# Optimization experiments

Hardware: AMD Instinct MI355X
Metric: run time of the kernel (lower is better)

## Reference

```python
import jax, jax.numpy as jnp
import numpy as np

N_SAMPLE = 1000
N_LATENT = 64
N_OUT = 64
BATCH = 65536


def setup_inputs() -> dict:
    key = jax.random.key(0)
    k_u, k_sid, k_A, k_off = jax.random.split(key, 4)
    u = jax.random.normal(k_u, (BATCH, N_LATENT), dtype=jnp.float32)
    sample_id = jax.random.randint(k_sid, (BATCH, 1), 0, N_SAMPLE, dtype=jnp.int64)
    amat_sample = jax.random.normal(k_A, (N_SAMPLE, N_LATENT, N_OUT), dtype=jnp.float32)
    offsets = jax.random.normal(k_off, (N_SAMPLE, N_OUT), dtype=jnp.float32)
    return {"u": u, "sample_id": sample_id, "amat_sample": amat_sample, "offsets": offsets}


def reference(u, sample_id, amat_sample, offsets):
    # sample_id: [B, 1] -> [B]
    sid = jnp.squeeze(sample_id, axis=-1).astype(jnp.int32)
    # Gather per-cell decoder matrix: [B, n_latent, n_out]
    As = amat_sample[sid]
    # Original detaches u before the matvec (gradient only flows via residual).
    u_sg = jax.lax.stop_gradient(u)
    # Batched matvec: (As * u[..., None]).sum(-2)
    z2 = jnp.einsum('bd,bdo->bo', u_sg, As)
    delta = z2 + offsets[sid]
    return u + delta
```

## Files before the change

kernel.cpp:

```cpp
#include <hip/hip_runtime.h>
#include <hip/hip_bf16.h>

#define N_LATENT 64
#define N_OUT    64
#define CAP      256
#define CSTRIDE  16
#define NWAVES   5
#define TPAD     68

typedef __attribute__((ext_vector_type(8))) _Float16 f16x8;
typedef __attribute__((ext_vector_type(4))) float    f32x4;

union U4H8 { uint4 u4; f16x8 h8; };

__global__ __launch_bounds__(256) void build_lists_kernel(
    const int* __restrict__ sid,
    int* __restrict__ cursor,
    int* __restrict__ list,
    int batch)
{
    const int i = blockIdx.x * blockDim.x + threadIdx.x;
    if (i < batch) {
        const int s = sid[i];
        const int p = atomicAdd(&cursor[s * CSTRIDE], 1);
        if (p < CAP) list[s * CAP + p] = i;
    }
}

__global__ __launch_bounds__(64 * NWAVES) void decoder_mfma_kernel(
    const float* __restrict__ u,
    const float* __restrict__ amat,
    const float* __restrict__ offsets,
    const int*   __restrict__ cursor,
    const int*   __restrict__ list,
    float*       __restrict__ out)
{
    __shared__ uint  Bf[8 * 64 * 4];
    __shared__ float Ot[NWAVES][16 * TPAD];

    const int s    = blockIdx.x;
    const int tid  = threadIdx.x;
    const int lane = tid & 63;
    const int wave = tid >> 6;

    int n = cursor[s * CSTRIDE];
    n = (n < CAP) ? n : CAP;
    if (n == 0) return;

    const float* __restrict__ Ag  = amat + (size_t)s * (N_LATENT * N_OUT);
    const int*   __restrict__ lst = list + s * CAP;

    for (int c = wave; c < 8; c += NWAVES) {
        const int kk  = c >> 2;
        const int nt  = c & 3;
        const int kb  = kk * 32 + (lane >> 4) * 8;
        const int col = nt * 16 + (lane & 15);
        U4H8 x;
#pragma unroll
        for (int j = 0; j < 8; ++j)
            x.h8[j] = (_Float16)Ag[(kb + j) * N_OUT + col];
        *((uint4*)&Bf[(c * 64 + lane) * 4]) = x.u4;
    }
    __syncthreads();

    const int tiles = (n + 15) >> 4;

    const float4 offv = *(const float4*)(offsets + (size_t)s * N_OUT + (lane & 15) * 4);

    float* __restrict__ myT = &Ot[wave][0];

    for (int t = wave; t < tiles; t += NWAVES) {
        const int ridx = t * 16 + (lane & 15);
        const int brow = lst[(ridx < n) ? ridx : 0];
        const float* __restrict__ up =
            u + (size_t)brow * N_LATENT + ((lane >> 4) * 8);
        f16x8 a0, a1;
        {
            const float4 p0 = *(const float4*)(up);
            const float4 p1 = *(const float4*)(up + 4);
            const float4 p2 = *(const float4*)(up + 32);
            const float4 p3 = *(const float4*)(up + 36);
            a0[0] = (_Float16)p0.x; a0[1] = (_Float16)p0.y;
            a0[2] = (_Float16)p0.z; a0[3] = (_Float16)p0.w;
            a0[4] = (_Float16)p1.x; a0[5] = (_Float16)p1.y;
            a0[6] = (_Float16)p1.z; a0[7] = (_Float16)p1.w;
            a1[0] = (_Float16)p2.x; a1[1] = (_Float16)p2.y;
            a1[2] = (_Float16)p2.z; a1[3] = (_Float16)p2.w;
            a1[4] = (_Float16)p3.x; a1[5] = (_Float16)p3.y;
            a1[6] = (_Float16)p3.z; a1[7] = (_Float16)p3.w;
        }

#pragma unroll
        for (int nt = 0; nt < 4; ++nt) {
            U4H8 b0, b1;
            b0.u4 = *((const uint4*)&Bf[((0 * 4 + nt) * 64 + lane) * 4]);
            b1.u4 = *((const uint4*)&Bf[((1 * 4 + nt) * 64 + lane) * 4]);
            f32x4 acc = {0.f, 0.f, 0.f, 0.f};
            acc = __builtin_amdgcn_mfma_f32_16x16x32_f16(a0, b0.h8, acc, 0, 0, 0);
            acc = __builtin_amdgcn_mfma_f32_16x16x32_f16(a1, b1.h8, acc, 0, 0, 0);

            const int col = nt * 16 + (lane & 15);
#pragma unroll
            for (int r = 0; r < 4; ++r)
                myT[((lane >> 4) * 4 + r) * TPAD + col] = acc[r];
        }
        asm volatile("s_waitcnt lgkmcnt(0)" ::: "memory");

#pragma unroll
        for (int p = 0; p < 4; ++p) {
            const int r2    = p * 4 + (lane >> 4);
            const int ridx2 = t * 16 + r2;
            if (ridx2 < n) {
                const int brow2 = lst[ridx2];
                const float* __restrict__ urow =
                    u + (size_t)brow2 * N_LATENT + (lane & 15) * 4;
                float* __restrict__ orow =
                    out + (size_t)brow2 * N_OUT + (lane & 15) * 4;
                const float4 uq = *(const float4*)urow;
                const float4 tv = *(const float4*)(myT + r2 * TPAD + (lane & 15) * 4);
                float4 o;
                o.x = uq.x + tv.x + offv.x;
                o.y = uq.y + tv.y + offv.y;
                o.z = uq.z + tv.z + offv.z;
                o.w = uq.w + tv.w + offv.w;
                *(float4*)orow = o;
            }
        }
    }
}

extern "C" void kernel_launch(void* const* d_in, const int* in_sizes, int n_in,
                              void* d_out, int out_size, void* d_ws, size_t ws_size,
                              hipStream_t stream)
{
    const float* u       = (const float*)d_in[0];
    const int*   sid     = (const int*)d_in[1];
    const float* amat    = (const float*)d_in[2];
    const float* offsets = (const float*)d_in[3];
    float*       out     = (float*)d_out;

    const int batch    = in_sizes[0] / N_LATENT;
    const int n_sample = in_sizes[2] / (N_LATENT * N_OUT);

    int* cursor = (int*)d_ws;
    int* list   = cursor + (size_t)n_sample * CSTRIDE;

    hipMemsetAsync(cursor, 0, (size_t)n_sample * CSTRIDE * sizeof(int), stream);

    build_lists_kernel<<<(batch + 255) / 256, 256, 0, stream>>>(
        sid, cursor, list, batch);

    decoder_mfma_kernel<<<n_sample, 64 * NWAVES, 0, stream>>>(
        u, amat, offsets, cursor, list, out);
}
```

Baseline: 25.70 us.

## Fuse list building into decoder kernel via per-block scan of sample ids

```diff
diff --git a/kernel.cpp b/kernel.cpp
--- a/kernel.cpp
+++ b/kernel.cpp
@@ -4,53 +4,39 @@
 #define N_LATENT 64
 #define N_OUT    64
 #define CAP      256
-#define CSTRIDE  16
-#define NWAVES   5
+#define NWAVES   8
 #define TPAD     68
+#define NTHR     (64 * NWAVES)
 
 typedef __attribute__((ext_vector_type(8))) _Float16 f16x8;
 typedef __attribute__((ext_vector_type(4))) float    f32x4;
 
 union U4H8 { uint4 u4; f16x8 h8; };
 
-__global__ __launch_bounds__(256) void build_lists_kernel(
-    const int* __restrict__ sid,
-    int* __restrict__ cursor,
-    int* __restrict__ list,
-    int batch)
-{
-    const int i = blockIdx.x * blockDim.x + threadIdx.x;
-    if (i < batch) {
-        const int s = sid[i];
-        const int p = atomicAdd(&cursor[s * CSTRIDE], 1);
-        if (p < CAP) list[s * CAP + p] = i;
-    }
-}
-
-__global__ __launch_bounds__(64 * NWAVES) void decoder_mfma_kernel(
+__global__ __launch_bounds__(NTHR) void decoder_scan_mfma_kernel(
     const float* __restrict__ u,
+    const int*   __restrict__ sid,
     const float* __restrict__ amat,
     const float* __restrict__ offsets,
-    const int*   __restrict__ cursor,
-    const int*   __restrict__ list,
-    float*       __restrict__ out)
+    float*       __restrict__ out,
+    int batch)
 {
     __shared__ uint  Bf[8 * 64 * 4];
     __shared__ float Ot[NWAVES][16 * TPAD];
+    __shared__ int   list[CAP];
+    __shared__ int   cnt;
 
     const int s    = blockIdx.x;
     const int tid  = threadIdx.x;
     const int lane = tid & 63;
     const int wave = tid >> 6;
 
-    int n = cursor[s * CSTRIDE];
-    n = (n < CAP) ? n : CAP;
-    if (n == 0) return;
+    const float* __restrict__ Ag = amat + (size_t)s * (N_LATENT * N_OUT);
 
-    const float* __restrict__ Ag  = amat + (size_t)s * (N_LATENT * N_OUT);
-    const int*   __restrict__ lst = list + s * CAP;
+    if (tid == 0) cnt = 0;
 
-    for (int c = wave; c < 8; c += NWAVES) {
+    {
+        const int c   = wave;
         const int kk  = c >> 2;
         const int nt  = c & 3;
         const int kb  = kk * 32 + (lane >> 4) * 8;
@@ -61,17 +47,33 @@
             x.h8[j] = (_Float16)Ag[(kb + j) * N_OUT + col];
         *((uint4*)&Bf[(c * 64 + lane) * 4]) = x.u4;
     }
+
+    {
+        const int4* __restrict__ sid4 = (const int4*)sid;
+        const int n4 = batch >> 2;
+        for (int i = tid; i < n4; i += NTHR) {
+            const int4 v = sid4[i];
+            const int rbase = 4 * i;
+            if (v.x == s) { int p = atomicAdd(&cnt, 1); if (p < CAP) list[p] = rbase;     }
+            if (v.y == s) { int p = atomicAdd(&cnt, 1); if (p < CAP) list[p] = rbase + 1; }
+            if (v.z == s) { int p = atomicAdd(&cnt, 1); if (p < CAP) list[p] = rbase + 2; }
+            if (v.w == s) { int p = atomicAdd(&cnt, 1); if (p < CAP) list[p] = rbase + 3; }
+        }
+    }
     __syncthreads();
+
+    int n = cnt;
+    n = (n < CAP) ? n : CAP;
+    if (n == 0) return;
 
     const int tiles = (n + 15) >> 4;
 
     const float4 offv = *(const float4*)(offsets + (size_t)s * N_OUT + (lane & 15) * 4);
-
     float* __restrict__ myT = &Ot[wave][0];
 
     for (int t = wave; t < tiles; t += NWAVES) {
         const int ridx = t * 16 + (lane & 15);
-        const int brow = lst[(ridx < n) ? ridx : 0];
+        const int brow = list[(ridx < n) ? ridx : 0];
         const float* __restrict__ up =
             u + (size_t)brow * N_LATENT + ((lane >> 4) * 8);
         f16x8 a0, a1;
@@ -111,7 +113,7 @@
             const int r2    = p * 4 + (lane >> 4);
             const int ridx2 = t * 16 + r2;
             if (ridx2 < n) {
-                const int brow2 = lst[ridx2];
+                const int brow2 = list[ridx2];
                 const float* __restrict__ urow =
                     u + (size_t)brow2 * N_LATENT + (lane & 15) * 4;
                 float* __restrict__ orow =
@@ -142,14 +144,6 @@
     const int batch    = in_sizes[0] / N_LATENT;
     const int n_sample = in_sizes[2] / (N_LATENT * N_OUT);
 
-    int* cursor = (int*)d_ws;
-    int* list   = cursor + (size_t)n_sample * CSTRIDE;
-
-    hipMemsetAsync(cursor, 0, (size_t)n_sample * CSTRIDE * sizeof(int), stream);
-
-    build_lists_kernel<<<(batch + 255) / 256, 256, 0, stream>>>(
-        sid, cursor, list, batch);
-
-    decoder_mfma_kernel<<<n_sample, 64 * NWAVES, 0, stream>>>(
-        u, amat, offsets, cursor, list, out);
+    decoder_scan_mfma_kernel<<<n_sample, NTHR, 0, stream>>>(
+        u, sid, amat, offsets, out, batch);
 }
```

Result: slower. 33.33 us (+29.7%).
